# Kernel optimization log

Hardware: AMD Instinct MI355X
Metric: run time of the kernel (lower is better)

## Reference

```python
import jax, jax.numpy as jnp
import numpy as np

B, S, V, E, Hd, O = 64, 512, 50000, 512, 1024, 10


def setup_inputs() -> dict:
    key = jax.random.key(0)
    ks = jax.random.split(key, 12)
    inp = {
        "inputs": jax.random.randint(ks[0], (B, S), 0, V),
        "weights": jax.random.normal(ks[1], (V, E), dtype=jnp.float32),
        "W_xr": jax.random.normal(ks[2], (E, Hd), dtype=jnp.float32) / np.sqrt(E),
        "W_hr": jax.random.normal(ks[3], (Hd, Hd), dtype=jnp.float32) / np.sqrt(Hd),
        "b_r": jnp.zeros((Hd,), dtype=jnp.float32),
        "W_xz": jax.random.normal(ks[4], (E, Hd), dtype=jnp.float32) / np.sqrt(E),
        "W_hz": jax.random.normal(ks[5], (Hd, Hd), dtype=jnp.float32) / np.sqrt(Hd),
        "b_z": jnp.ones((Hd,), dtype=jnp.float32),
        "W_xc": jax.random.normal(ks[6], (E, Hd), dtype=jnp.float32) / np.sqrt(E),
        "W_hc": jax.random.normal(ks[7], (Hd, Hd), dtype=jnp.float32) / np.sqrt(Hd),
        "b_c": jnp.zeros((Hd,), dtype=jnp.float32),
        "W_hq": jax.random.normal(ks[8], (Hd, O), dtype=jnp.float32) / np.sqrt(Hd),
        "b_q": jnp.zeros((O,), dtype=jnp.float32),
    }
    return inp


def reference(inputs, weights, W_xr, W_hr, b_r, W_xz, W_hz, b_z,
              W_xc, W_hc, b_c, W_hq, b_q):
    # embed: [B, S, E] -> time-major [S, B, E]
    xs = jnp.swapaxes(weights[inputs], 0, 1)

    def step(H, X):
        r = jax.nn.sigmoid(X @ W_xr + H @ W_hr + b_r)
        z = jax.nn.sigmoid(X @ W_xz + H @ W_hz + b_z)
        h = jnp.tanh(X @ W_xc + (H * r) @ W_hc + b_c)
        H_new = z * H + (1.0 - z) * h
        return H_new, None

    H0 = jnp.zeros((inputs.shape[0], W_hr.shape[0]), dtype=weights.dtype)
    H, _ = jax.lax.scan(step, H0, xs)
    return jax.nn.softmax(H @ W_hq + b_q, axis=1)
```

## Files before the change

### kernel.cpp

```cpp
#include <hip/hip_runtime.h>
#include <stdint.h>

#define S_LEN 512
#define B_SZ  64
#define E_DIM 512
#define HD    1024
#define NGATE 3072
#define O_DIM 10

typedef __attribute__((ext_vector_type(4))) float f32x4;
typedef __attribute__((ext_vector_type(8))) short bf16x8;

__device__ __forceinline__ float bf2f(unsigned short u) {
  union { unsigned int i; float f; } c; c.i = ((unsigned int)u) << 16; return c.f;
}
__device__ __forceinline__ unsigned short f2bf(float f) {
  union { float f; unsigned int i; } c; c.f = f;
  unsigned int u = c.i;
  return (unsigned short)((u + 0x7fffu + ((u >> 16) & 1u)) >> 16);
}
__device__ __forceinline__ float sigmoid_fast(float x) { return 1.0f / (1.0f + __expf(-x)); }
__device__ __forceinline__ float tanh_fast(float x) {
  float a = fabsf(x);
  float e = __expf(2.0f * a);
  return copysignf(1.0f - 2.0f / (e + 1.0f), x);
}
__device__ __forceinline__ f32x4 mfma16(bf16x8 a, bf16x8 b, f32x4 c) {
  return __builtin_amdgcn_mfma_f32_16x16x32_bf16(a, b, c, 0, 0, 0);
}
__device__ __forceinline__ unsigned long long ld_u64_agent(const unsigned long long* p) {
  return __hip_atomic_load(p, __ATOMIC_RELAXED, __HIP_MEMORY_SCOPE_AGENT);
}
__device__ __forceinline__ void st_u64_agent(unsigned long long* p, unsigned long long v) {
  __hip_atomic_store(p, v, __ATOMIC_RELAXED, __HIP_MEMORY_SCOPE_AGENT);
}
__device__ __forceinline__ unsigned int ld_u32_agent(const unsigned int* p) {
  return __hip_atomic_load(p, __ATOMIC_RELAXED, __HIP_MEMORY_SCOPE_AGENT);
}
__device__ __forceinline__ void st_u32_agent(unsigned int* p, unsigned int v) {
  __hip_atomic_store(p, v, __ATOMIC_RELAXED, __HIP_MEMORY_SCOPE_AGENT);
}

#define SLOT_STRIDE 64
#define OFF_HB2   0
#define OFF_RH2   262144
#define OFF_HF    393216
#define OFF_SLOTS 655360
#define OFF_WR    1704960
#define OFF_WZ    3802112
#define OFF_WC    5899264
#define OFF_WX    7996416
#define OFF_XP    11142144

__global__ void convert_kernel(const float* __restrict__ Whr, const float* __restrict__ Whz,
                               const float* __restrict__ Whc,
                               const float* __restrict__ Wxr, const float* __restrict__ Wxz,
                               const float* __restrict__ Wxc,
                               unsigned short* __restrict__ Wr_swz, unsigned short* __restrict__ Wz_swz,
                               unsigned short* __restrict__ Wc_swz, unsigned short* __restrict__ Wx_swz) {
  long idx = (long)blockIdx.x * blockDim.x + threadIdx.x;
  const long NH = (long)HD * HD;
  if (idx < 3 * NH) {
    int m = (int)(idx >> 20);
    int t = (int)(idx & (NH - 1));
    int k = t >> 10, j = t & 1023;
    const float* src = (m == 0) ? Whr : (m == 1) ? Whz : Whc;
    unsigned short* dst = (m == 0) ? Wr_swz : (m == 1) ? Wz_swz : Wc_swz;
    int jt = j >> 4, n = j & 15, kt = k >> 5, q = (k >> 3) & 3, i = k & 7;
    dst[((long)(jt * 32 + kt) * 64 + (q * 16 + n)) * 8 + i] = f2bf(src[(long)k * HD + j]);
  } else {
    long t = idx - 3 * NH;
    if (t < (long)E_DIM * NGATE) {
      int e  = (int)(t / NGATE);
      int jg = (int)(t - (long)e * NGATE);
      int jt = jg >> 4, n = jg & 15, kt = e >> 5, q = (e >> 3) & 3, i = e & 7;
      int gate = jg >> 10, jj = jg & 1023;
      const float* src = (gate == 0) ? Wxr : (gate == 1) ? Wxz : Wxc;
      Wx_swz[((long)(jt * 16 + kt) * 64 + (q * 16 + n)) * 8 + i] = f2bf(src[(long)e * HD + jj]);
    }
  }
}

__launch_bounds__(256, 2)
__global__ void embed_kernel(const int* __restrict__ tokens,
                             const float* __restrict__ Emb,
                             const unsigned short* __restrict__ Wx_swz,
                             const float* __restrict__ b_r, const float* __restrict__ b_z,
                             const float* __restrict__ b_c,
                             unsigned short* __restrict__ Xp) {
  __shared__ unsigned short xl[B_SZ * E_DIM];
  const int s = blockIdx.y;
  const int slab = blockIdx.x;
  const int tid = threadIdx.x;
  for (int it = 0; it < 32; ++it) {
    int task = tid + 256 * it;
    int row = task >> 7;
    int f = task & 127;
    int tok = tokens[row * S_LEN + s];
    float4 v = *(const float4*)(Emb + (long)tok * E_DIM + f * 4);
    int sw = (f >> 1) ^ (row & 7);
    unsigned short* p = xl + row * E_DIM + sw * 8 + (f & 1) * 4;
    p[0] = f2bf(v.x); p[1] = f2bf(v.y); p[2] = f2bf(v.z); p[3] = f2bf(v.w);
  }
  __syncthreads();
  const int lane = tid & 63, wave = tid >> 6;
  const int n = lane & 15, q = lane >> 4;
  const int jt_glob = slab * 4 + wave;
  f32x4 acc[4];
  #pragma unroll
  for (int bt = 0; bt < 4; ++bt) { acc[bt][0]=0.f; acc[bt][1]=0.f; acc[bt][2]=0.f; acc[bt][3]=0.f; }
  for (int kt = 0; kt < 16; ++kt) {
    bf16x8 bfrag = *(const bf16x8*)(Wx_swz + ((long)(jt_glob * 16 + kt) * 64 + lane) * 8);
    #pragma unroll
    for (int bt = 0; bt < 4; ++bt) {
      int row = bt * 16 + n;
      int chunk = (kt * 4 + q) ^ (row & 7);
      bf16x8 afrag = *(const bf16x8*)(xl + row * E_DIM + chunk * 8);
      acc[bt] = mfma16(afrag, bfrag, acc[bt]);
    }
  }
  const int jglob = jt_glob * 16 + n;
  const int gate = jglob >> 10, jj = jglob & 1023;
  const float bias = (gate == 0 ? b_r : gate == 1 ? b_z : b_c)[jj];
  #pragma unroll
  for (int bt = 0; bt < 4; ++bt) {
    unsigned int lo = (unsigned)f2bf(acc[bt][0] + bias) | ((unsigned)f2bf(acc[bt][1] + bias) << 16);
    unsigned int hi = (unsigned)f2bf(acc[bt][2] + bias) | ((unsigned)f2bf(acc[bt][3] + bias) << 16);
    uint2 pk; pk.x = lo; pk.y = hi;
    *(uint2*)(Xp + (((long)s * 4 + bt) * NGATE + jglob) * 16 + q * 4) = pk;
  }
}

__launch_bounds__(256, 1)
__global__ void gru_kernel(const unsigned short* __restrict__ Xp,
                           const unsigned short* __restrict__ Wr_swz,
                           const unsigned short* __restrict__ Wz_swz,
                           const unsigned short* __restrict__ Wc_swz,
                           unsigned short* __restrict__ Hb2,
                           float* __restrict__ Hf,
                           unsigned short* __restrict__ rh2,
                           unsigned int* __restrict__ slots) {
  __shared__ float red[4][6][256];
  __shared__ float zbuf[2][256];
  __shared__ unsigned short ldsT[2][256];
  __shared__ float hmaster[16 * 32];

  const int tid = threadIdx.x;
  const int lane = tid & 63, w = tid >> 6;
  const int n = lane & 15, q = lane >> 4;
  const int blk = blockIdx.x;
  const int g  = blk & 3;
  const int bh = blk >> 2;
  const int row_t = lane >> 2, word_t = lane & 3;

  bf16x8 wr_reg[2][8], wz_reg[2][8], wc_reg[2][8];
  #pragma unroll
  for (int jt = 0; jt < 2; ++jt)
    #pragma unroll
    for (int t = 0; t < 8; ++t) {
      long o = ((long)((2 * bh + jt) * 32 + w * 8 + t)) * 512 + lane * 8;
      wr_reg[jt][t] = *(const bf16x8*)(Wr_swz + o);
      wz_reg[jt][t] = *(const bf16x8*)(Wz_swz + o);
      wc_reg[jt][t] = *(const bf16x8*)(Wc_swz + o);
    }
  for (int i = tid; i < 512; i += 256) hmaster[i] = 0.f;
  __syncthreads();

  unsigned int* gslots = slots + g * 64 * SLOT_STRIDE;
  unsigned int* myflag = gslots + (bh * 2 + w) * SLOT_STRIDE;
  const unsigned int* pollp =
      gslots + (((w * 8 + (lane >> 1)) * 2) + (lane & 1)) * SLOT_STRIDE;

  unsigned long long* rh_u64 = (unsigned long long*)rh2;
  unsigned long long* hb_u64 = (unsigned long long*)Hb2;

  const int gate_w = w >> 1, jt_w = w & 1;
  const long xp_stride = (long)4 * NGATE * 16;
  const unsigned short* xp1_p = Xp + (((long)g * NGATE) + gate_w * HD + bh * 32 + jt_w * 16 + n) * 16 + q * 4;
  const unsigned short* xpc_p = Xp + (((long)g * NGATE) + 2 * HD + bh * 32 + w * 16 + n) * 16 + q * 4;

  uint2 xp1 = *(const uint2*)xp1_p;
  uint2 xpc; xpc.x = 0; xpc.y = 0;
  if (w < 2) xpc = *(const uint2*)xpc_p;

  const long my_off = (long)(g * 32 + bh) * 128 + row_t * 8 + w * 4 + word_t;
  const long ld_off = (long)n * 8 + q * 2;
  const long grp128 = (long)g * 32 * 128;

  unsigned long long a0[8], a1[8];
  #pragma unroll
  for (int t = 0; t < 8; ++t) { a0[t] = 0ull; a1[t] = 0ull; }

  int cur = 0;
  unsigned int seq = 1;

  for (int s = 0; s < S_LEN; ++s) {
    f32x4 aR0, aR1;
    aR0[0]=0.f;aR0[1]=0.f;aR0[2]=0.f;aR0[3]=0.f; aR1 = aR0;
    #pragma unroll
    for (int t = 0; t < 8; ++t) {
      union { unsigned long long u[2]; bf16x8 v; } af;
      af.u[0] = a0[t]; af.u[1] = a1[t];
      aR0 = mfma16(af.v, wr_reg[0][t], aR0);
      aR1 = mfma16(af.v, wr_reg[1][t], aR1);
    }
    *(f32x4*)&red[w][0][lane * 4] = aR0;
    *(f32x4*)&red[w][1][lane * 4] = aR1;
    __syncthreads();
    if (w < 2) {
      f32x4 acc = *(const f32x4*)&red[0][w][lane * 4];
      #pragma unroll
      for (int k = 1; k < 4; ++k) { f32x4 p = *(const f32x4*)&red[k][w][lane * 4]; acc += p; }
      #pragma unroll
      for (int r_ = 0; r_ < 4; ++r_) {
        float xpv = bf2f((unsigned short)(((r_ < 2) ? xp1.x : xp1.y) >> ((r_ & 1) * 16)));
        float rv = sigmoid_fast(acc[r_] + xpv);
        ldsT[w][(q * 4 + r_) * 16 + n] = f2bf(rv * hmaster[(q * 4 + r_) * 32 + w * 16 + n]);
      }
      asm volatile("s_waitcnt lgkmcnt(0)" ::: "memory");
      unsigned long long pay = *(const unsigned long long*)(&ldsT[w][row_t * 16 + word_t * 4]);
      st_u64_agent(rh_u64 + my_off, pay);
      asm volatile("s_waitcnt vmcnt(0)" ::: "memory");
      if (lane == 0) st_u32_agent(myflag, seq);
    }
    f32x4 aZ0, aZ1;
    aZ0[0]=0.f;aZ0[1]=0.f;aZ0[2]=0.f;aZ0[3]=0.f; aZ1 = aZ0;
    #pragma unroll
    for (int t = 0; t < 8; ++t) {
      union { unsigned long long u[2]; bf16x8 v; } af;
      af.u[0] = a0[t]; af.u[1] = a1[t];
      aZ0 = mfma16(af.v, wz_reg[0][t], aZ0);
      aZ1 = mfma16(af.v, wz_reg[1][t], aZ1);
    }
    *(f32x4*)&red[w][2][lane * 4] = aZ0;
    *(f32x4*)&red[w][3][lane * 4] = aZ1;
    if (lane < 16) { while (ld_u32_agent(pollp) < seq) {} }
    asm volatile("" ::: "memory");
    unsigned long long c0[8], c1[8];
    #pragma unroll
    for (int t = 0; t < 8; ++t) {
      const unsigned long long* p =
          (const unsigned long long*)rh2 + grp128 + (long)(w * 8 + t) * 128 + ld_off;
      c0[t] = ld_u64_agent(p);
      c1[t] = ld_u64_agent(p + 1);
    }
    __syncthreads();
    if (w >= 2) {
      f32x4 accz = *(const f32x4*)&red[0][w][lane * 4];
      #pragma unroll
      for (int k = 1; k < 4; ++k) { f32x4 p = *(const f32x4*)&red[k][w][lane * 4]; accz += p; }
      #pragma unroll
      for (int r_ = 0; r_ < 4; ++r_) {
        float xpv = bf2f((unsigned short)(((r_ < 2) ? xp1.x : xp1.y) >> ((r_ & 1) * 16)));
        zbuf[w - 2][(q * 4 + r_) * 16 + n] = sigmoid_fast(accz[r_] + xpv);
      }
    }
    f32x4 cA, cB;
    cA[0]=0.f;cA[1]=0.f;cA[2]=0.f;cA[3]=0.f; cB = cA;
    #pragma unroll
    for (int t = 0; t < 8; ++t) {
      union { unsigned long long u[2]; bf16x8 v; } af;
      af.u[0] = c0[t]; af.u[1] = c1[t];
      cA = mfma16(af.v, wc_reg[0][t], cA);
      cB = mfma16(af.v, wc_reg[1][t], cB);
    }
    *(f32x4*)&red[w][4][lane * 4] = cA;
    *(f32x4*)&red[w][5][lane * 4] = cB;
    __syncthreads();
    if (w < 2) {
      f32x4 acc2 = *(const f32x4*)&red[0][4 + w][lane * 4];
      #pragma unroll
      for (int k = 1; k < 4; ++k) { f32x4 p = *(const f32x4*)&red[k][4 + w][lane * 4]; acc2 += p; }
      #pragma unroll
      for (int r_ = 0; r_ < 4; ++r_) {
        float xpv = bf2f((unsigned short)(((r_ < 2) ? xpc.x : xpc.y) >> ((r_ & 1) * 16)));
        float cv = tanh_fast(acc2[r_] + xpv);
        float z  = zbuf[w][(q * 4 + r_) * 16 + n];
        float h0 = hmaster[(q * 4 + r_) * 32 + w * 16 + n];
        float hn = z * h0 + (1.0f - z) * cv;
        hmaster[(q * 4 + r_) * 32 + w * 16 + n] = hn;
        ldsT[w][(q * 4 + r_) * 16 + n] = f2bf(hn);
        if (s == S_LEN - 1)
          Hf[(long)(g * 16 + q * 4 + r_) * HD + bh * 32 + w * 16 + n] = hn;
      }
      asm volatile("s_waitcnt lgkmcnt(0)" ::: "memory");
      unsigned long long pay = *(const unsigned long long*)(&ldsT[w][row_t * 16 + word_t * 4]);
      st_u64_agent(hb_u64 + (long)(cur ^ 1) * 16384 + my_off, pay);
      asm volatile("s_waitcnt vmcnt(0)" ::: "memory");
      if (lane == 0) st_u32_agent(myflag, seq + 1);
    }
    if (s < S_LEN - 1) {
      uint2 xp1n = *(const uint2*)(xp1_p + (long)(s + 1) * xp_stride);
      uint2 xpcn; xpcn.x = 0; xpcn.y = 0;
      if (w < 2) xpcn = *(const uint2*)(xpc_p + (long)(s + 1) * xp_stride);
      if (lane < 16) { while (ld_u32_agent(pollp) < seq + 1) {} }
      asm volatile("" ::: "memory");
      const unsigned long long* hb =
          (const unsigned long long*)Hb2 + (long)(cur ^ 1) * 16384 + grp128;
      #pragma unroll
      for (int t = 0; t < 8; ++t) {
        const unsigned long long* p = hb + (long)(w * 8 + t) * 128 + ld_off;
        a0[t] = ld_u64_agent(p);
        a1[t] = ld_u64_agent(p + 1);
      }
      xp1 = xp1n;
      if (w < 2) xpc = xpcn;
    }
    seq += 2;
    cur ^= 1;
  }
}

__global__ void logits_kernel(const float* __restrict__ Hf, const float* __restrict__ Whq,
                              const float* __restrict__ bq, float* __restrict__ out) {
  const int b = blockIdx.x;
  const int lane = threadIdx.x;
  float acc[O_DIM];
  #pragma unroll
  for (int o = 0; o < O_DIM; ++o) acc[o] = 0.f;
  for (int k = lane; k < HD; k += 64) {
    float h = Hf[(long)b * HD + k];
    #pragma unroll
    for (int o = 0; o < O_DIM; ++o) acc[o] += h * Whq[(long)k * O_DIM + o];
  }
  #pragma unroll
  for (int o = 0; o < O_DIM; ++o) {
    #pragma unroll
    for (int off = 32; off > 0; off >>= 1) acc[o] += __shfl_down(acc[o], off, 64);
  }
  if (lane == 0) {
    float lg[O_DIM], m = -1e30f, sum = 0.f;
    #pragma unroll
    for (int o = 0; o < O_DIM; ++o) { lg[o] = acc[o] + bq[o]; m = fmaxf(m, lg[o]); }
    #pragma unroll
    for (int o = 0; o < O_DIM; ++o) { lg[o] = __expf(lg[o] - m); sum += lg[o]; }
    float inv = 1.0f / sum;
    #pragma unroll
    for (int o = 0; o < O_DIM; ++o) out[(long)b * O_DIM + o] = lg[o] * inv;
  }
}

extern "C" void kernel_launch(void* const* d_in, const int* in_sizes, int n_in,
                              void* d_out, int out_size, void* d_ws, size_t ws_size,
                              hipStream_t stream) {
  const int*   tokens = (const int*)d_in[0];
  const float* Emb = (const float*)d_in[1];
  const float* Wxr = (const float*)d_in[2];
  const float* Whr = (const float*)d_in[3];
  const float* br  = (const float*)d_in[4];
  const float* Wxz = (const float*)d_in[5];
  const float* Whz = (const float*)d_in[6];
  const float* bz  = (const float*)d_in[7];
  const float* Wxc = (const float*)d_in[8];
  const float* Whc = (const float*)d_in[9];
  const float* bc  = (const float*)d_in[10];
  const float* Whq = (const float*)d_in[11];
  const float* bq  = (const float*)d_in[12];

  char* ws = (char*)d_ws;
  unsigned short* Hb2    = (unsigned short*)(ws + OFF_HB2);
  unsigned short* rh2    = (unsigned short*)(ws + OFF_RH2);
  float*          Hf     = (float*)(ws + OFF_HF);
  unsigned int*   slots  = (unsigned int*)(ws + OFF_SLOTS);
  unsigned short* Wr_swz = (unsigned short*)(ws + OFF_WR);
  unsigned short* Wz_swz = (unsigned short*)(ws + OFF_WZ);
  unsigned short* Wc_swz = (unsigned short*)(ws + OFF_WC);
  unsigned short* Wx_swz = (unsigned short*)(ws + OFF_WX);
  unsigned short* Xp     = (unsigned short*)(ws + OFF_XP);

  hipMemsetAsync(ws + OFF_SLOTS, 0, 65536, stream);

  convert_kernel<<<18432, 256, 0, stream>>>(Whr, Whz, Whc, Wxr, Wxz, Wxc,
                                            Wr_swz, Wz_swz, Wc_swz, Wx_swz);
  embed_kernel<<<dim3(48, S_LEN), 256, 0, stream>>>(tokens, Emb, Wx_swz, br, bz, bc, Xp);
  gru_kernel<<<128, 256, 0, stream>>>(Xp, Wr_swz, Wz_swz, Wc_swz,
                                      Hb2, Hf, rh2, slots);
  logits_kernel<<<B_SZ, 64, 0, stream>>>(Hf, Whq, bq, (float*)d_out);
}
```

Baseline: 3.553 ms.

## Spread gate epilogue across all four waves with direct 32-bit stores

```diff
diff --git a/kernel.cpp b/kernel.cpp
--- a/kernel.cpp
+++ b/kernel.cpp
@@ -30,9 +30,6 @@
 }
 __device__ __forceinline__ unsigned long long ld_u64_agent(const unsigned long long* p) {
   return __hip_atomic_load(p, __ATOMIC_RELAXED, __HIP_MEMORY_SCOPE_AGENT);
-}
-__device__ __forceinline__ void st_u64_agent(unsigned long long* p, unsigned long long v) {
-  __hip_atomic_store(p, v, __ATOMIC_RELAXED, __HIP_MEMORY_SCOPE_AGENT);
 }
 __device__ __forceinline__ unsigned int ld_u32_agent(const unsigned int* p) {
   return __hip_atomic_load(p, __ATOMIC_RELAXED, __HIP_MEMORY_SCOPE_AGENT);
@@ -141,8 +138,7 @@
                            unsigned short* __restrict__ rh2,
                            unsigned int* __restrict__ slots) {
   __shared__ float red[4][6][256];
-  __shared__ float zbuf[2][256];
-  __shared__ unsigned short ldsT[2][256];
+  __shared__ float zbuf[16 * 32];
   __shared__ float hmaster[16 * 32];
 
   const int tid = threadIdx.x;
@@ -151,7 +147,13 @@
   const int blk = blockIdx.x;
   const int g  = blk & 3;
   const int bh = blk >> 2;
-  const int row_t = lane >> 2, word_t = lane & 3;
+
+  const int rr = lane >> 4;
+  const int m  = lane & 15;
+  const int prow = 4 * w + rr;
+  const int pc = 2 * m;
+  const int t0 = pc >> 4;
+  const int n0 = pc & 15;
 
   bf16x8 wr_reg[2][8], wz_reg[2][8], wc_reg[2][8];
   #pragma unroll
@@ -166,26 +168,27 @@
   for (int i = tid; i < 512; i += 256) hmaster[i] = 0.f;
   __syncthreads();
 
-  unsigned int* gslots = slots + g * 64 * SLOT_STRIDE;
-  unsigned int* myflag = gslots + (bh * 2 + w) * SLOT_STRIDE;
+  unsigned int* gslots = slots + g * 128 * SLOT_STRIDE;
+  unsigned int* myflag = gslots + (bh * 4 + w) * SLOT_STRIDE;
   const unsigned int* pollp =
-      gslots + (((w * 8 + (lane >> 1)) * 2) + (lane & 1)) * SLOT_STRIDE;
-
-  unsigned long long* rh_u64 = (unsigned long long*)rh2;
-  unsigned long long* hb_u64 = (unsigned long long*)Hb2;
-
-  const int gate_w = w >> 1, jt_w = w & 1;
-  const long xp_stride = (long)4 * NGATE * 16;
-  const unsigned short* xp1_p = Xp + (((long)g * NGATE) + gate_w * HD + bh * 32 + jt_w * 16 + n) * 16 + q * 4;
-  const unsigned short* xpc_p = Xp + (((long)g * NGATE) + 2 * HD + bh * 32 + w * 16 + n) * 16 + q * 4;
-
-  uint2 xp1 = *(const uint2*)xp1_p;
-  uint2 xpc; xpc.x = 0; xpc.y = 0;
-  if (w < 2) xpc = *(const uint2*)xpc_p;
-
-  const long my_off = (long)(g * 32 + bh) * 128 + row_t * 8 + w * 4 + word_t;
-  const long ld_off = (long)n * 8 + q * 2;
-  const long grp128 = (long)g * 32 * 128;
+      gslots + ((w * 8 + (lane >> 2)) * 4 + (lane & 3)) * SLOT_STRIDE;
+
+  const long xp_step = (long)4 * NGATE * 16;
+  const unsigned short* xr_p = Xp + ((long)g * NGATE + bh * 32 + pc) * 16 + prow;
+  const unsigned short* xc_p = Xp + ((long)g * NGATE + 2 * HD + bh * 32 + pc) * 16 + prow;
+  const unsigned short* xz_p = Xp + ((long)g * NGATE + HD + bh * 32 + (w & 1) * 16 + n) * 16 + q * 4;
+
+  unsigned short xr0 = xr_p[0],  xr1 = xr_p[16];
+  unsigned short xc0 = xc_p[0],  xc1 = xc_p[16];
+  uint2 xz; xz.x = 0; xz.y = 0;
+  if (w >= 2) xz = *(const uint2*)xz_p;
+
+  const long my32 = (long)(g * 32 + bh) * 256 + (long)prow * 16 + m;
+  const long ld64 = (long)n * 8 + q * 2;
+  const long grp64 = (long)g * 4096;
+
+  unsigned int* rh_u32 = (unsigned int*)rh2;
+  unsigned int* hb_u32 = (unsigned int*)Hb2;
 
   unsigned long long a0[8], a1[8];
   #pragma unroll
@@ -207,19 +210,17 @@
     *(f32x4*)&red[w][0][lane * 4] = aR0;
     *(f32x4*)&red[w][1][lane * 4] = aR1;
     __syncthreads();
-    if (w < 2) {
-      f32x4 acc = *(const f32x4*)&red[0][w][lane * 4];
-      #pragma unroll
-      for (int k = 1; k < 4; ++k) { f32x4 p = *(const f32x4*)&red[k][w][lane * 4]; acc += p; }
-      #pragma unroll
-      for (int r_ = 0; r_ < 4; ++r_) {
-        float xpv = bf2f((unsigned short)(((r_ < 2) ? xp1.x : xp1.y) >> ((r_ & 1) * 16)));
-        float rv = sigmoid_fast(acc[r_] + xpv);
-        ldsT[w][(q * 4 + r_) * 16 + n] = f2bf(rv * hmaster[(q * 4 + r_) * 32 + w * 16 + n]);
-      }
-      asm volatile("s_waitcnt lgkmcnt(0)" ::: "memory");
-      unsigned long long pay = *(const unsigned long long*)(&ldsT[w][row_t * 16 + word_t * 4]);
-      st_u64_agent(rh_u64 + my_off, pay);
+    {
+      float v0 = 0.f, v1 = 0.f;
+      #pragma unroll
+      for (int k = 0; k < 4; ++k) {
+        v0 += red[k][t0][(w * 16 + n0) * 4 + rr];
+        v1 += red[k][t0][(w * 16 + n0 + 1) * 4 + rr];
+      }
+      float r0 = sigmoid_fast(v0 + bf2f(xr0)) * hmaster[prow * 32 + pc];
+      float r1 = sigmoid_fast(v1 + bf2f(xr1)) * hmaster[prow * 32 + pc + 1];
+      unsigned int pay = (unsigned)f2bf(r0) | ((unsigned)f2bf(r1) << 16);
+      st_u32_agent(rh_u32 + my32, pay);
       asm volatile("s_waitcnt vmcnt(0)" ::: "memory");
       if (lane == 0) st_u32_agent(myflag, seq);
     }
@@ -234,25 +235,26 @@
     }
     *(f32x4*)&red[w][2][lane * 4] = aZ0;
     *(f32x4*)&red[w][3][lane * 4] = aZ1;
-    if (lane < 16) { while (ld_u32_agent(pollp) < seq) {} }
+    if (lane < 32) { while (ld_u32_agent(pollp) < seq) {} }
     asm volatile("" ::: "memory");
-    unsigned long long c0[8], c1[8];
+    unsigned long long rA[8], rB[8];
     #pragma unroll
     for (int t = 0; t < 8; ++t) {
       const unsigned long long* p =
-          (const unsigned long long*)rh2 + grp128 + (long)(w * 8 + t) * 128 + ld_off;
-      c0[t] = ld_u64_agent(p);
-      c1[t] = ld_u64_agent(p + 1);
+          (const unsigned long long*)rh2 + grp64 + (long)(w * 8 + t) * 128 + ld64;
+      rA[t] = ld_u64_agent(p);
+      rB[t] = ld_u64_agent(p + 1);
     }
     __syncthreads();
     if (w >= 2) {
-      f32x4 accz = *(const f32x4*)&red[0][w][lane * 4];
-      #pragma unroll
-      for (int k = 1; k < 4; ++k) { f32x4 p = *(const f32x4*)&red[k][w][lane * 4]; accz += p; }
+      const int tz = w - 2;
+      f32x4 accz = *(const f32x4*)&red[0][2 + tz][lane * 4];
+      #pragma unroll
+      for (int k = 1; k < 4; ++k) { f32x4 p = *(const f32x4*)&red[k][2 + tz][lane * 4]; accz += p; }
       #pragma unroll
       for (int r_ = 0; r_ < 4; ++r_) {
-        float xpv = bf2f((unsigned short)(((r_ < 2) ? xp1.x : xp1.y) >> ((r_ & 1) * 16)));
-        zbuf[w - 2][(q * 4 + r_) * 16 + n] = sigmoid_fast(accz[r_] + xpv);
+        float xpv = bf2f((unsigned short)(((r_ < 2) ? xz.x : xz.y) >> ((r_ & 1) * 16)));
+        zbuf[(q * 4 + r_) * 32 + tz * 16 + n] = sigmoid_fast(accz[r_] + xpv);
       }
     }
     f32x4 cA, cB;
@@ -260,51 +262,55 @@
     #pragma unroll
     for (int t = 0; t < 8; ++t) {
       union { unsigned long long u[2]; bf16x8 v; } af;
-      af.u[0] = c0[t]; af.u[1] = c1[t];
+      af.u[0] = rA[t]; af.u[1] = rB[t];
       cA = mfma16(af.v, wc_reg[0][t], cA);
       cB = mfma16(af.v, wc_reg[1][t], cB);
     }
     *(f32x4*)&red[w][4][lane * 4] = cA;
     *(f32x4*)&red[w][5][lane * 4] = cB;
     __syncthreads();
-    if (w < 2) {
-      f32x4 acc2 = *(const f32x4*)&red[0][4 + w][lane * 4];
-      #pragma unroll
-      for (int k = 1; k < 4; ++k) { f32x4 p = *(const f32x4*)&red[k][4 + w][lane * 4]; acc2 += p; }
-      #pragma unroll
-      for (int r_ = 0; r_ < 4; ++r_) {
-        float xpv = bf2f((unsigned short)(((r_ < 2) ? xpc.x : xpc.y) >> ((r_ & 1) * 16)));
-        float cv = tanh_fast(acc2[r_] + xpv);
-        float z  = zbuf[w][(q * 4 + r_) * 16 + n];
-        float h0 = hmaster[(q * 4 + r_) * 32 + w * 16 + n];
-        float hn = z * h0 + (1.0f - z) * cv;
-        hmaster[(q * 4 + r_) * 32 + w * 16 + n] = hn;
-        ldsT[w][(q * 4 + r_) * 16 + n] = f2bf(hn);
-        if (s == S_LEN - 1)
-          Hf[(long)(g * 16 + q * 4 + r_) * HD + bh * 32 + w * 16 + n] = hn;
-      }
-      asm volatile("s_waitcnt lgkmcnt(0)" ::: "memory");
-      unsigned long long pay = *(const unsigned long long*)(&ldsT[w][row_t * 16 + word_t * 4]);
-      st_u64_agent(hb_u64 + (long)(cur ^ 1) * 16384 + my_off, pay);
+    {
+      float v0 = 0.f, v1 = 0.f;
+      #pragma unroll
+      for (int k = 0; k < 4; ++k) {
+        v0 += red[k][4 + t0][(w * 16 + n0) * 4 + rr];
+        v1 += red[k][4 + t0][(w * 16 + n0 + 1) * 4 + rr];
+      }
+      float cv0 = tanh_fast(v0 + bf2f(xc0));
+      float cv1 = tanh_fast(v1 + bf2f(xc1));
+      float z0 = zbuf[prow * 32 + pc],     z1 = zbuf[prow * 32 + pc + 1];
+      float h0 = hmaster[prow * 32 + pc],  h1 = hmaster[prow * 32 + pc + 1];
+      float hn0 = z0 * h0 + (1.0f - z0) * cv0;
+      float hn1 = z1 * h1 + (1.0f - z1) * cv1;
+      hmaster[prow * 32 + pc]     = hn0;
+      hmaster[prow * 32 + pc + 1] = hn1;
+      if (s == S_LEN - 1) {
+        Hf[(long)(g * 16 + prow) * HD + bh * 32 + pc]     = hn0;
+        Hf[(long)(g * 16 + prow) * HD + bh * 32 + pc + 1] = hn1;
+      }
+      unsigned int pay = (unsigned)f2bf(hn0) | ((unsigned)f2bf(hn1) << 16);
+      st_u32_agent(hb_u32 + (long)(cur ^ 1) * 32768 + my32, pay);
       asm volatile("s_waitcnt vmcnt(0)" ::: "memory");
       if (lane == 0) st_u32_agent(myflag, seq + 1);
     }
     if (s < S_LEN - 1) {
-      uint2 xp1n = *(const uint2*)(xp1_p + (long)(s + 1) * xp_stride);
-      uint2 xpcn; xpcn.x = 0; xpcn.y = 0;
-      if (w < 2) xpcn = *(const uint2*)(xpc_p + (long)(s + 1) * xp_stride);
-      if (lane < 16) { while (ld_u32_agent(pollp) < seq + 1) {} }
+      const unsigned short* xr_s = xr_p + (long)(s + 1) * xp_step;
+      const unsigned short* xc_s = xc_p + (long)(s + 1) * xp_step;
+      unsigned short xr0n = xr_s[0], xr1n = xr_s[16];
+      unsigned short xc0n = xc_s[0], xc1n = xc_s[16];
+      uint2 xzn; xzn.x = 0; xzn.y = 0;
+      if (w >= 2) xzn = *(const uint2*)(xz_p + (long)(s + 1) * xp_step);
+      if (lane < 32) { while (ld_u32_agent(pollp) < seq + 1) {} }
       asm volatile("" ::: "memory");
       const unsigned long long* hb =
-          (const unsigned long long*)Hb2 + (long)(cur ^ 1) * 16384 + grp128;
+          (const unsigned long long*)Hb2 + (long)(cur ^ 1) * 16384 + grp64;
       #pragma unroll
       for (int t = 0; t < 8; ++t) {
-        const unsigned long long* p = hb + (long)(w * 8 + t) * 128 + ld_off;
+        const unsigned long long* p = hb + (long)(w * 8 + t) * 128 + ld64;
         a0[t] = ld_u64_agent(p);
         a1[t] = ld_u64_agent(p + 1);
       }
-      xp1 = xp1n;
-      if (w < 2) xpc = xpcn;
+      xr0 = xr0n; xr1 = xr1n; xc0 = xc0n; xc1 = xc1n; xz = xzn;
     }
     seq += 2;
     cur ^= 1;
@@ -368,7 +374,7 @@
   unsigned short* Wx_swz = (unsigned short*)(ws + OFF_WX);
   unsigned short* Xp     = (unsigned short*)(ws + OFF_XP);
 
-  hipMemsetAsync(ws + OFF_SLOTS, 0, 65536, stream);
+  hipMemsetAsync(ws + OFF_SLOTS, 0, 131072, stream);
 
   convert_kernel<<<18432, 256, 0, stream>>>(Whr, Whz, Whc, Wxr, Wxz, Wxc,
                                             Wr_swz, Wz_swz, Wc_swz, Wx_swz);
```

Measured after the change: 3.272 ms. 1.09x faster.
